# Performance work log

Measured on AMD Instinct MI355X. Metric: run time of the kernel, lower is better.

## Reference

```python
import jax, jax.numpy as jnp
import numpy as np

IN_CH = 128
HIDDEN = 256
CHUNK = 4096
EPS = 1e-8  # F.cosine_similarity default eps


def setup_inputs() -> dict:
    key = jax.random.key(0)
    ks = jax.random.split(key, 10)
    N, E, P = 8192, 262144, 65536
    x = jax.random.normal(ks[0], (N, IN_CH), dtype=jnp.float32)
    edge_index = jax.random.randint(ks[1], (2, E), 0, N, dtype=jnp.int64)
    edge_pairs = jax.random.randint(ks[2], (P, 2), 0, N, dtype=jnp.int64)
    input_dim = 2 * IN_CH + IN_CH + IN_CH + IN_CH + 1 + 3  # 644
    h2 = HIDDEN // 2
    def lin(k, fan_in, fan_out):
        bound = 1.0 / np.sqrt(fan_in)
        kw, kb = jax.random.split(k)
        W = jax.random.uniform(kw, (fan_in, fan_out), minval=-bound, maxval=bound, dtype=jnp.float32)
        b = jax.random.uniform(kb, (fan_out,), minval=-bound, maxval=bound, dtype=jnp.float32)
        return W, b
    W1, b1 = lin(ks[3], input_dim, HIDDEN)
    W2, b2 = lin(ks[4], HIDDEN, h2)
    W3, b3 = lin(ks[5], h2, 1)
    return {"x": x, "edge_index": edge_index, "edge_pairs": edge_pairs,
            "W1": W1, "b1": b1, "W2": W2, "b2": b2, "W3": W3, "b3": b3}


def _forward(x, edge_index, edge_pairs, W1, b1, W2, b2, W3, b3):
    N = x.shape[0]
    # dense adjacency cache (matches DenseHeuristicMixin._ensure_graph_cache)
    adj = jnp.zeros((N, N), dtype=jnp.float32).at[edge_index[0], edge_index[1]].set(1.0)
    diag = jnp.arange(N)
    adj = adj.at[diag, diag].set(0.0)
    deg = adj.sum(axis=1)
    inv_log_deg = jnp.where(deg > 1, 1.0 / jnp.log(jnp.where(deg > 1, deg, 2.0)), 0.0)
    inv_deg = jnp.where(deg > 0, 1.0 / jnp.where(deg > 0, deg, 1.0), 0.0)

    P = edge_pairs.shape[0]
    pairs = edge_pairs.reshape(P // CHUNK, CHUNK, 2)

    def chunk_body(carry, pc):
        u, v = pc[:, 0], pc[:, 1]
        xu, xv = x[u], x[v]                          # [C, d]
        # cosine similarity (eps-clamped denominator, as in torch)
        nu = jnp.sqrt(jnp.sum(xu * xu, axis=1))
        nv = jnp.sqrt(jnp.sum(xv * xv, axis=1))
        cos = jnp.sum(xu * xv, axis=1) / jnp.maximum(nu * nv, EPS)
        # dense heuristic features: [C, N] adjacency-row products
        common = adj[u] * adj[v]
        cn = common.sum(axis=1)
        aa = common @ inv_log_deg
        ra = common @ inv_deg
        feats = jnp.concatenate(
            [xu, xv, xu * xv, jnp.abs(xu - xv), xu + xv,
             cos[:, None], cn[:, None], aa[:, None], ra[:, None]], axis=1)
        h = jax.nn.relu(feats @ W1 + b1)  # dropout is identity in eval mode
        h = jax.nn.relu(h @ W2 + b2)
        s = (h @ W3 + b3)[:, 0]
        return carry, s

    _, scores = jax.lax.scan(chunk_body, None, pairs)
    return scores.reshape(-1)


def reference(x, edge_index, edge_pairs, W1, b1, W2, b2, W3, b3):
    return _forward(x, edge_index, edge_pairs, W1, b1, W2, b2, W3, b3)
```

## Files before the change

### kernel.cpp

```cpp
#include <hip/hip_runtime.h>
#include <hip/hip_bf16.h>

#define IN_CH   128
#define HIDDEN  256
#define H2DIM   128
#define KS1     17
#define KS2     8
#define NT1     16
#define NT2     8
#define FSTR    296
#define H1S     264
#define CAP     64
#define T1PACK  (NT1*KS1*64)
#define T2PACK  (NT2*KS2*64)

typedef short short8v __attribute__((ext_vector_type(8)));
typedef float f32x4   __attribute__((ext_vector_type(4)));

__device__ __forceinline__ ushort f2bf(float f) {
  union { float f; uint32_t u; } c; c.f = f;
  uint32_t u = c.u + 0x7FFFu + ((c.u >> 16) & 1u);
  return (ushort)(u >> 16);
}
__device__ __forceinline__ float bf2f(ushort h) {
  union { uint32_t u; float f; } c; c.u = ((uint32_t)h) << 16;
  return c.f;
}
__device__ __forceinline__ float bfLo(uint32_t u) { return bf2f((ushort)(u & 0xffffu)); }
__device__ __forceinline__ float bfHi(uint32_t u) { return bf2f((ushort)(u >> 16)); }
__device__ __forceinline__ uint32_t pk2(float a, float b) {
  __hip_bfloat162 h = __float22bfloat162_rn(make_float2(a, b));
  union { __hip_bfloat162 h; uint32_t u; } c; c.h = h;
  return c.u;
}

__global__ void k_prep(const float* __restrict__ W1, const float* __restrict__ W2,
                       ushort* __restrict__ w1p, ushort* __restrict__ w2p,
                       uint32_t* __restrict__ bits, int nwords) {
  int t = blockIdx.x * blockDim.x + threadIdx.x;
  if (t < T1PACK) {
    int l = t & 63;
    int rest = t >> 6;
    int ks = rest % KS1;
    int nt = rest / KS1;
    int n  = nt * 16 + (l & 15);
    int k0 = ks * 32 + (l >> 4) * 8;
    short8v v;
    #pragma unroll
    for (int j = 0; j < 8; ++j) {
      int k = k0 + j;
      float val;
      if (k < 128)      val = W1[(size_t)k * HIDDEN + n] + W1[(size_t)(512 + k) * HIDDEN + n];
      else if (k < 256) val = W1[(size_t)k * HIDDEN + n] + W1[(size_t)(384 + k) * HIDDEN + n];
      else if (k < 512) val = W1[(size_t)k * HIDDEN + n];
      else if (k < 516) val = W1[(size_t)(k + 128) * HIDDEN + n];
      else              val = 0.f;
      v[j] = (short)f2bf(val);
    }
    *(short8v*)(w1p + (size_t)t * 8) = v;
  } else if (t < T1PACK + T2PACK) {
    int t2 = t - T1PACK;
    int l = t2 & 63;
    int rest = t2 >> 6;
    int ks = rest % KS2;
    int nt = rest / KS2;
    int n  = nt * 16 + (l & 15);
    int k0 = ks * 32 + (l >> 4) * 8;
    short8v v;
    #pragma unroll
    for (int j = 0; j < 8; ++j)
      v[j] = (short)f2bf(W2[(size_t)(k0 + j) * H2DIM + n]);
    *(short8v*)(w2p + (size_t)t2 * 8) = v;
  }
  int stride = gridDim.x * blockDim.x;
  for (int i = t; i < nwords; i += stride) bits[i] = 0u;
}

__global__ void k_build_adj(const int* __restrict__ ei, int E, int roww,
                            uint32_t* __restrict__ bits) {
  int e = blockIdx.x * blockDim.x + threadIdx.x;
  if (e >= E) return;
  int u = ei[e];
  int v = ei[E + e];
  if (u == v) return;
  atomicOr((unsigned int*)&bits[(size_t)u * roww + (v >> 5)], 1u << (v & 31));
}

__global__ void k_node_lists(const uint32_t* __restrict__ bits, const float* __restrict__ x,
                             int nnodes, int roww,
                             float* __restrict__ invlog, float* __restrict__ invdeg,
                             int* __restrict__ deg, float* __restrict__ nrm,
                             ushort* __restrict__ adjl, ushort* __restrict__ xbf) {
  int node = blockIdx.x * (blockDim.x >> 6) + (threadIdx.x >> 6);
  int lane = threadIdx.x & 63;
  if (node >= nnodes) return;
  const uint32_t* row = bits + (size_t)node * roww;
  uint32_t wd[4];
  int c = 0;
  #pragma unroll
  for (int j = 0; j < 4; ++j) { wd[j] = row[lane * 4 + j]; c += __popc(wd[j]); }
  int sum = c;
  #pragma unroll
  for (int off = 1; off < 64; off <<= 1) {
    int t = __shfl_up(sum, off);
    if (lane >= off) sum += t;
  }
  int excl = sum - c;
  int total = __shfl(sum, 63);
  ushort* lst = adjl + (size_t)node * CAP;
  int pos = excl;
  #pragma unroll
  for (int j = 0; j < 4; ++j) {
    uint32_t m = wd[j];
    int base = (lane * 4 + j) * 32;
    while (m) {
      int b = __ffs(m) - 1;
      if (pos < CAP) lst[pos] = (ushort)(base + b);
      ++pos;
      m &= m - 1;
    }
  }
  float2 xa = *(const float2*)(x + (size_t)node * IN_CH + 2 * lane);
  *(uint32_t*)(xbf + (size_t)node * IN_CH + 2 * lane) = pk2(xa.x, xa.y);
  float ss = xa.x * xa.x + xa.y * xa.y;
  #pragma unroll
  for (int off = 32; off; off >>= 1) ss += __shfl_xor(ss, off);
  if (lane == 0) {
    deg[node] = total;
    float d = (float)total;
    invlog[node] = (total > 1) ? 1.0f / logf(d) : 0.0f;
    invdeg[node] = (total > 0) ? 1.0f / d : 0.0f;
    nrm[node] = sqrtf(ss);
  }
}

__global__ __launch_bounds__(512, 4) void k_mlp10(
    const ushort* __restrict__ xbf, const int* __restrict__ pairs,
    const uint32_t* __restrict__ bits, int roww,
    const int* __restrict__ deg, const float* __restrict__ nrm,
    const float* __restrict__ invlog, const float* __restrict__ invdeg,
    const ushort* __restrict__ adjl,
    const ushort* __restrict__ w1p, const float* __restrict__ b1,
    const ushort* __restrict__ w2p, const float* __restrict__ b2,
    const float* __restrict__ W3, const float* __restrict__ b3,
    float* __restrict__ out, int P)
{
  __shared__ ushort feats[64 * FSTR];
  __shared__ float outacc[64];
  __shared__ int us[64], vs[64];

  int tid = threadIdx.x;
  int pb = blockIdx.x * 64;
  int w  = tid >> 6, l = tid & 63;
  int pg = l >> 3, g = l & 7;
  int lr = l & 15;
  int lk = l >> 4;

  if (tid < 64) {
    int2 pr = ((const int2*)pairs)[pb + tid];
    us[tid] = pr.x; vs[tid] = pr.y;
    outacc[tid] = b3[0];
  }
  __syncthreads();

  int p = w * 8 + pg;
  int u = us[p], v = vs[p];
  ushort* fpR = feats + p * FSTR;
  ushort* fp  = fpR + g * 16;

  {
    const ushort* xup = xbf + (size_t)u * IN_CH + g * 16;
    const ushort* xvp = xbf + (size_t)v * IN_CH + g * 16;
    uint4 A0 = *(const uint4*)(xup);
    uint4 A1 = *(const uint4*)(xup + 8);
    uint4 B0 = *(const uint4*)(xvp);
    uint4 B1 = *(const uint4*)(xvp + 8);
    *(uint4*)(fp)       = A0;
    *(uint4*)(fp + 8)   = A1;
    *(uint4*)(fp + 128) = B0;
    *(uint4*)(fp + 136) = B1;
    float suv = bfLo(A0.x)*bfLo(B0.x) + bfHi(A0.x)*bfHi(B0.x)
              + bfLo(A0.y)*bfLo(B0.y) + bfHi(A0.y)*bfHi(B0.y)
              + bfLo(A0.z)*bfLo(B0.z) + bfHi(A0.z)*bfHi(B0.z)
              + bfLo(A0.w)*bfLo(B0.w) + bfHi(A0.w)*bfHi(B0.w)
              + bfLo(A1.x)*bfLo(B1.x) + bfHi(A1.x)*bfHi(B1.x)
              + bfLo(A1.y)*bfLo(B1.y) + bfHi(A1.y)*bfHi(B1.y)
              + bfLo(A1.z)*bfLo(B1.z) + bfHi(A1.z)*bfHi(B1.z)
              + bfLo(A1.w)*bfLo(B1.w) + bfHi(A1.w)*bfHi(B1.w);
    suv += __shfl_xor(suv, 1);
    suv += __shfl_xor(suv, 2);
    suv += __shfl_xor(suv, 4);
    if (g == 0) fpR[256] = f2bf(suv / fmaxf(nrm[u] * nrm[v], 1e-8f));
    if (g < 7) *(uint2*)(fpR + 260 + 4 * g) = make_uint2(0u, 0u);
  }

  {
    int sdmin[8], snbs[8];
    uint32_t swrd[8];
    bool sfall = false;
    #pragma unroll
    for (int pp = 0; pp < 8; ++pp) {
      int ps_ = w * 8 + pp;
      int uu = us[ps_], vv = vs[ps_];
      int du = deg[uu], dv = deg[vv];
      int nu = adjl[(size_t)uu * CAP + l];
      int nv = adjl[(size_t)vv * CAP + l];
      bool ule = du <= dv;
      sdmin[pp] = ule ? du : dv;
      int o  = ule ? vv : uu;
      int nb = (ule ? nu : nv) & 8191;
      snbs[pp] = nb;
      swrd[pp] = bits[(size_t)o * roww + (nb >> 5)];
      sfall |= (sdmin[pp] > CAP);
    }
    if (!sfall) {
      #pragma unroll
      for (int pp = 0; pp < 8; ++pp) {
        bool h = (l < sdmin[pp]) && ((swrd[pp] >> (snbs[pp] & 31)) & 1u);
        unsigned long long mask = __ballot(h);
        float cnv = (float)__popcll(mask);
        float aa = 0.f, ra = 0.f;
        if (mask) {
          float il = 0.f, ig = 0.f;
          if (h) { il = invlog[snbs[pp]]; ig = invdeg[snbs[pp]]; }
          while (mask) {
            int ln = __ffsll(mask) - 1;
            aa += __shfl(il, ln);
            ra += __shfl(ig, ln);
            mask &= mask - 1;
          }
        }
        if (l == 0) {
          ushort* fq = feats + (w * 8 + pp) * FSTR;
          fq[257] = f2bf(cnv); fq[258] = f2bf(aa); fq[259] = f2bf(ra);
        }
      }
    } else {
      for (int pp = 0; pp < 8; ++pp) {
        int ps_ = w * 8 + pp;
        int uu = us[ps_], vv = vs[ps_];
        float cnL = 0.f, aaL = 0.f, raL = 0.f;
        const uint32_t* ru = bits + (size_t)uu * roww;
        const uint32_t* rv = bits + (size_t)vv * roww;
        for (int wd = l; wd < roww; wd += 64) {
          uint32_t c = ru[wd] & rv[wd];
          cnL += (float)__popc(c);
          while (c) {
            int bb = __ffs(c) - 1;
            int idx = wd * 32 + bb;
            aaL += invlog[idx]; raL += invdeg[idx];
            c &= c - 1;
          }
        }
        #pragma unroll
        for (int off = 32; off; off >>= 1) {
          cnL += __shfl_xor(cnL, off);
          aaL += __shfl_xor(aaL, off);
          raL += __shfl_xor(raL, off);
        }
        if (l == 0) {
          ushort* fq = feats + (w * 8 + pp) * FSTR;
          fq[257] = f2bf(cnL); fq[258] = f2bf(aaL); fq[259] = f2bf(raL);
        }
      }
    }
  }
  __syncthreads();

  f32x4 acc[4][2];
  #pragma unroll
  for (int m = 0; m < 4; ++m)
    #pragma unroll
    for (int i = 0; i < 2; ++i) acc[m][i] = (f32x4){0.f, 0.f, 0.f, 0.f};

  const ushort* aB = feats + lr * FSTR + lk * 8;
  const ushort* bW = w1p + (size_t)(w * 2) * KS1 * 512 + l * 8;

  {
    short8v bf[2][2];
    #pragma unroll
    for (int i = 0; i < 2; ++i)
      bf[0][i] = *(const short8v*)(bW + (size_t)(i * KS1) * 512);
    #pragma unroll
    for (int ks = 0; ks < 8; ++ks) {
      int cur = ks & 1, nxt = cur ^ 1;
      if (ks + 1 < 8) {
        #pragma unroll
        for (int i = 0; i < 2; ++i)
          bf[nxt][i] = *(const short8v*)(bW + (size_t)(i * KS1 + ks + 1) * 512);
      }
      short8v am[4];
      #pragma unroll
      for (int m = 0; m < 4; ++m)
        am[m] = *(const short8v*)(aB + m * 16 * FSTR + ks * 32);
      #pragma unroll
      for (int i = 0; i < 2; ++i)
        #pragma unroll
        for (int m = 0; m < 4; ++m)
          acc[m][i] = __builtin_amdgcn_mfma_f32_16x16x32_bf16(am[m], bf[cur][i], acc[m][i], 0, 0, 0);
    }
  }
  __syncthreads();

  {
    uint4 A0 = *(uint4*)(fp);
    uint4 A1 = *(uint4*)(fp + 8);
    uint4 B0 = *(uint4*)(fp + 128);
    uint4 B1 = *(uint4*)(fp + 136);
    uint4 P0, P1, D0, D1;
    #define PD(Au, Bu, Pu, Du)                                                 \
      {                                                                        \
        float alo = bfLo(Au), ahi = bfHi(Au);                                  \
        float blo = bfLo(Bu), bhi = bfHi(Bu);                                  \
        Pu = pk2(alo * blo, ahi * bhi);                                        \
        Du = pk2(fabsf(alo - blo), fabsf(ahi - bhi));                          \
      }
    PD(A0.x, B0.x, P0.x, D0.x) PD(A0.y, B0.y, P0.y, D0.y)
    PD(A0.z, B0.z, P0.z, D0.z) PD(A0.w, B0.w, P0.w, D0.w)
    PD(A1.x, B1.x, P1.x, D1.x) PD(A1.y, B1.y, P1.y, D1.y)
    PD(A1.z, B1.z, P1.z, D1.z) PD(A1.w, B1.w, P1.w, D1.w)
    #undef PD
    *(uint4*)(fp)       = P0;
    *(uint4*)(fp + 8)   = P1;
    *(uint4*)(fp + 128) = D0;
    *(uint4*)(fp + 136) = D1;
  }
  __syncthreads();

  {
    short8v bf[2][2];
    #pragma unroll
    for (int i = 0; i < 2; ++i)
      bf[0][i] = *(const short8v*)(bW + (size_t)(i * KS1 + 8) * 512);
    #pragma unroll
    for (int ks = 8; ks < KS1; ++ks) {
      int cur = ks & 1, nxt = cur ^ 1;
      if (ks + 1 < KS1) {
        #pragma unroll
        for (int i = 0; i < 2; ++i)
          bf[nxt][i] = *(const short8v*)(bW + (size_t)(i * KS1 + ks + 1) * 512);
      }
      short8v am[4];
      #pragma unroll
      for (int m = 0; m < 4; ++m)
        am[m] = *(const short8v*)(aB + m * 16 * FSTR + (ks - 8) * 32);
      #pragma unroll
      for (int i = 0; i < 2; ++i)
        #pragma unroll
        for (int m = 0; m < 4; ++m)
          acc[m][i] = __builtin_amdgcn_mfma_f32_16x16x32_bf16(am[m], bf[cur][i], acc[m][i], 0, 0, 0);
    }
  }

  uint32_t h1r[2][8];
  #pragma unroll
  for (int i = 0; i < 2; ++i) {
    float bias = b1[(w * 2 + i) * 16 + lr];
    #pragma unroll
    for (int m = 0; m < 4; ++m) {
      float v0 = fmaxf(acc[m][i][0] + bias, 0.f);
      float v1 = fmaxf(acc[m][i][1] + bias, 0.f);
      float v2 = fmaxf(acc[m][i][2] + bias, 0.f);
      float v3 = fmaxf(acc[m][i][3] + bias, 0.f);
      h1r[i][m * 2]     = pk2(v0, v1);
      h1r[i][m * 2 + 1] = pk2(v2, v3);
    }
  }
  __syncthreads();

  ushort* h1 = feats;
  #pragma unroll
  for (int i = 0; i < 2; ++i) {
    int col = (w * 2 + i) * 16 + lr;
    #pragma unroll
    for (int m = 0; m < 4; ++m) {
      int row0 = m * 16 + lk * 4;
      h1[(row0)     * H1S + col] = (ushort)(h1r[i][m * 2]);
      h1[(row0 + 1) * H1S + col] = (ushort)(h1r[i][m * 2] >> 16);
      h1[(row0 + 2) * H1S + col] = (ushort)(h1r[i][m * 2 + 1]);
      h1[(row0 + 3) * H1S + col] = (ushort)(h1r[i][m * 2 + 1] >> 16);
    }
  }
  __syncthreads();

  f32x4 acc2[4];
  #pragma unroll
  for (int m = 0; m < 4; ++m) acc2[m] = (f32x4){0.f, 0.f, 0.f, 0.f};

  const ushort* aB2 = h1 + lr * H1S + lk * 8;
  const ushort* bW2 = w2p + (size_t)w * KS2 * 512 + l * 8;

  short8v b2f[2];
  b2f[0] = *(const short8v*)(bW2);

  #pragma unroll
  for (int ks = 0; ks < KS2; ++ks) {
    int cur = ks & 1, nxt = cur ^ 1;
    if (ks + 1 < KS2)
      b2f[nxt] = *(const short8v*)(bW2 + (size_t)(ks + 1) * 512);
    #pragma unroll
    for (int m = 0; m < 4; ++m) {
      short8v am = *(const short8v*)(aB2 + m * 16 * H1S + ks * 32);
      acc2[m] = __builtin_amdgcn_mfma_f32_16x16x32_bf16(am, b2f[cur], acc2[m], 0, 0, 0);
    }
  }

  {
    int col = w * 16 + lr;
    float bias = b2[col];
    float w3v = W3[col];
    #pragma unroll
    for (int m = 0; m < 4; ++m) {
      #pragma unroll
      for (int r = 0; r < 4; ++r) {
        float h = fmaxf(acc2[m][r] + bias, 0.f) * w3v;
        h += __shfl_xor(h, 1);
        h += __shfl_xor(h, 2);
        h += __shfl_xor(h, 4);
        h += __shfl_xor(h, 8);
        if (lr == 0) atomicAdd(&outacc[m * 16 + lk * 4 + r], h);
      }
    }
  }
  __syncthreads();

  if (tid < 64) out[pb + tid] = outacc[tid];
}

extern "C" void kernel_launch(void* const* d_in, const int* in_sizes, int n_in,
                              void* d_out, int out_size, void* d_ws, size_t ws_size,
                              hipStream_t stream) {
  const float* x     = (const float*)d_in[0];
  const int*   ei    = (const int*)d_in[1];
  const int*   pairs = (const int*)d_in[2];
  const float* W1    = (const float*)d_in[3];
  const float* b1    = (const float*)d_in[4];
  const float* W2    = (const float*)d_in[5];
  const float* b2    = (const float*)d_in[6];
  const float* W3    = (const float*)d_in[7];
  const float* b3    = (const float*)d_in[8];
  float* out = (float*)d_out;

  int N = in_sizes[0] / IN_CH;
  int E = in_sizes[1] / 2;
  int P = in_sizes[2] / 2;
  int roww = (N + 31) >> 5;

  char* wsb = (char*)d_ws;
  uint32_t* bits = (uint32_t*)wsb;                       size_t off = (size_t)N * roww * 4;
  float* invlog  = (float*)(wsb + off);                  off += (size_t)N * 4;
  float* invdeg  = (float*)(wsb + off);                  off += (size_t)N * 4;
  int*   deg     = (int*)(wsb + off);                    off += (size_t)N * 4;
  float* nrm     = (float*)(wsb + off);                  off += (size_t)N * 4;
  ushort* adjl   = (ushort*)(wsb + off);                 off += (size_t)N * CAP * 2;
  ushort* xbf    = (ushort*)(wsb + off);                 off += (size_t)N * IN_CH * 2;
  ushort* w1pack = (ushort*)(wsb + off);                 off += (size_t)T1PACK * 8 * 2;
  ushort* w2pack = (ushort*)(wsb + off);                 off += (size_t)T2PACK * 8 * 2;

  int nwords = N * roww;
  k_prep<<<1024, 256, 0, stream>>>(W1, W2, w1pack, w2pack, bits, nwords);
  k_build_adj<<<(E + 255) / 256, 256, 0, stream>>>(ei, E, roww, bits);
  k_node_lists<<<(N + 3) / 4, 256, 0, stream>>>(bits, x, N, roww, invlog, invdeg, deg, nrm, adjl, xbf);
  k_mlp10<<<P / 64, 512, 0, stream>>>(xbf, pairs, bits, roww, deg, nrm, invlog, invdeg, adjl,
                                      w1pack, b1, w2pack, b2, W3, b3, out, P);
}
```

Baseline: 79.23 us.

## Intersect sorted neighbor lists via warp binary search, pack node scalars into float2

Common-neighbor features now come from intersecting the two sorted adjacency lists inside a wavefront with a shuffle-based binary search when both degrees fit the cap, which avoids the random bitmap word gathers. The bitmap probe remains as a middle fallback and a full bitmap scan as the last resort. Per-node degree and norm, and the two inverse-degree terms, are packed into float2 arrays so each needs one load instead of two. The per-pair loop is no longer unrolled across 8 pairs, which reduces batching of the global loads.

```diff
diff --git a/kernel.cpp b/kernel.cpp
--- a/kernel.cpp
+++ b/kernel.cpp
@@ -88,8 +88,7 @@
 
 __global__ void k_node_lists(const uint32_t* __restrict__ bits, const float* __restrict__ x,
                              int nnodes, int roww,
-                             float* __restrict__ invlog, float* __restrict__ invdeg,
-                             int* __restrict__ deg, float* __restrict__ nrm,
+                             float2* __restrict__ dn, float2* __restrict__ nodeinv,
                              ushort* __restrict__ adjl, ushort* __restrict__ xbf) {
   int node = blockIdx.x * (blockDim.x >> 6) + (threadIdx.x >> 6);
   int lane = threadIdx.x & 63;
@@ -126,19 +125,18 @@
   #pragma unroll
   for (int off = 32; off; off >>= 1) ss += __shfl_xor(ss, off);
   if (lane == 0) {
-    deg[node] = total;
     float d = (float)total;
-    invlog[node] = (total > 1) ? 1.0f / logf(d) : 0.0f;
-    invdeg[node] = (total > 0) ? 1.0f / d : 0.0f;
-    nrm[node] = sqrtf(ss);
-  }
-}
-
-__global__ __launch_bounds__(512, 4) void k_mlp10(
+    dn[node] = make_float2(d, sqrtf(ss));
+    float il = (total > 1) ? 1.0f / logf(d) : 0.0f;
+    float ig = (total > 0) ? 1.0f / d : 0.0f;
+    nodeinv[node] = make_float2(il, ig);
+  }
+}
+
+__global__ __launch_bounds__(512, 4) void k_mlp11(
     const ushort* __restrict__ xbf, const int* __restrict__ pairs,
     const uint32_t* __restrict__ bits, int roww,
-    const int* __restrict__ deg, const float* __restrict__ nrm,
-    const float* __restrict__ invlog, const float* __restrict__ invdeg,
+    const float2* __restrict__ dn, const float2* __restrict__ nodeinv,
     const ushort* __restrict__ adjl,
     const ushort* __restrict__ w1p, const float* __restrict__ b1,
     const ushort* __restrict__ w2p, const float* __restrict__ b2,
@@ -190,79 +188,89 @@
     suv += __shfl_xor(suv, 1);
     suv += __shfl_xor(suv, 2);
     suv += __shfl_xor(suv, 4);
-    if (g == 0) fpR[256] = f2bf(suv / fmaxf(nrm[u] * nrm[v], 1e-8f));
+    if (g == 0) {
+      float nu = dn[u].y, nv = dn[v].y;
+      fpR[256] = f2bf(suv / fmaxf(nu * nv, 1e-8f));
+    }
     if (g < 7) *(uint2*)(fpR + 260 + 4 * g) = make_uint2(0u, 0u);
   }
 
-  {
-    int sdmin[8], snbs[8];
-    uint32_t swrd[8];
-    bool sfall = false;
-    #pragma unroll
-    for (int pp = 0; pp < 8; ++pp) {
-      int ps_ = w * 8 + pp;
-      int uu = us[ps_], vv = vs[ps_];
-      int du = deg[uu], dv = deg[vv];
-      int nu = adjl[(size_t)uu * CAP + l];
-      int nv = adjl[(size_t)vv * CAP + l];
-      bool ule = du <= dv;
-      sdmin[pp] = ule ? du : dv;
-      int o  = ule ? vv : uu;
-      int nb = (ule ? nu : nv) & 8191;
-      snbs[pp] = nb;
-      swrd[pp] = bits[(size_t)o * roww + (nb >> 5)];
-      sfall |= (sdmin[pp] > CAP);
-    }
-    if (!sfall) {
-      #pragma unroll
-      for (int pp = 0; pp < 8; ++pp) {
-        bool h = (l < sdmin[pp]) && ((swrd[pp] >> (snbs[pp] & 31)) & 1u);
-        unsigned long long mask = __ballot(h);
-        float cnv = (float)__popcll(mask);
-        float aa = 0.f, ra = 0.f;
-        if (mask) {
-          float il = 0.f, ig = 0.f;
-          if (h) { il = invlog[snbs[pp]]; ig = invdeg[snbs[pp]]; }
-          while (mask) {
-            int ln = __ffsll(mask) - 1;
-            aa += __shfl(il, ln);
-            ra += __shfl(ig, ln);
-            mask &= mask - 1;
-          }
+  for (int pp = 0; pp < 8; ++pp) {
+    int ps_ = w * 8 + pp;
+    int uu = us[ps_], vv = vs[ps_];
+    int du = (int)dn[uu].x, dv = (int)dn[vv].x;
+    bool ule = du <= dv;
+    int sn = ule ? uu : vv, on = ule ? vv : uu;
+    int ds = ule ? du : dv, dl = ule ? dv : du;
+    float cnv, aa = 0.f, ra = 0.f;
+    if (dl <= CAP) {
+      int a = adjl[(size_t)sn * CAP + l];
+      int b = adjl[(size_t)on * CAP + l];
+      int pos = 0;
+      #pragma unroll
+      for (int st = 32; st; st >>= 1) {
+        int cand = pos + st;
+        int bv = __shfl(b, cand - 1);
+        if (cand <= dl && bv < a) pos = cand;
+      }
+      int bp = __shfl(b, pos);
+      bool hit = (l < ds) && (pos < dl) && (bp == a);
+      unsigned long long mask = __ballot(hit);
+      cnv = (float)__popcll(mask);
+      if (mask) {
+        float il = 0.f, ig = 0.f;
+        if (hit) { float2 nv = nodeinv[a]; il = nv.x; ig = nv.y; }
+        while (mask) {
+          int ln = __ffsll(mask) - 1;
+          aa += __shfl(il, ln);
+          ra += __shfl(ig, ln);
+          mask &= mask - 1;
         }
-        if (l == 0) {
-          ushort* fq = feats + (w * 8 + pp) * FSTR;
-          fq[257] = f2bf(cnv); fq[258] = f2bf(aa); fq[259] = f2bf(ra);
+      }
+    } else if (ds <= CAP) {
+      bool hit = false; int nb = 0;
+      if (l < ds) {
+        nb = adjl[(size_t)sn * CAP + l];
+        hit = (bits[(size_t)on * roww + (nb >> 5)] >> (nb & 31)) & 1u;
+      }
+      unsigned long long mask = __ballot(hit);
+      cnv = (float)__popcll(mask);
+      if (mask) {
+        float il = 0.f, ig = 0.f;
+        if (hit) { float2 nv = nodeinv[nb]; il = nv.x; ig = nv.y; }
+        while (mask) {
+          int ln = __ffsll(mask) - 1;
+          aa += __shfl(il, ln);
+          ra += __shfl(ig, ln);
+          mask &= mask - 1;
         }
       }
     } else {
-      for (int pp = 0; pp < 8; ++pp) {
-        int ps_ = w * 8 + pp;
-        int uu = us[ps_], vv = vs[ps_];
-        float cnL = 0.f, aaL = 0.f, raL = 0.f;
-        const uint32_t* ru = bits + (size_t)uu * roww;
-        const uint32_t* rv = bits + (size_t)vv * roww;
-        for (int wd = l; wd < roww; wd += 64) {
-          uint32_t c = ru[wd] & rv[wd];
-          cnL += (float)__popc(c);
-          while (c) {
-            int bb = __ffs(c) - 1;
-            int idx = wd * 32 + bb;
-            aaL += invlog[idx]; raL += invdeg[idx];
-            c &= c - 1;
-          }
+      float cnL = 0.f, aaL = 0.f, raL = 0.f;
+      const uint32_t* ru = bits + (size_t)uu * roww;
+      const uint32_t* rv = bits + (size_t)vv * roww;
+      for (int wd = l; wd < roww; wd += 64) {
+        uint32_t c = ru[wd] & rv[wd];
+        cnL += (float)__popc(c);
+        while (c) {
+          int bb = __ffs(c) - 1;
+          int idx = wd * 32 + bb;
+          float2 nv = nodeinv[idx];
+          aaL += nv.x; raL += nv.y;
+          c &= c - 1;
         }
-        #pragma unroll
-        for (int off = 32; off; off >>= 1) {
-          cnL += __shfl_xor(cnL, off);
-          aaL += __shfl_xor(aaL, off);
-          raL += __shfl_xor(raL, off);
-        }
-        if (l == 0) {
-          ushort* fq = feats + (w * 8 + pp) * FSTR;
-          fq[257] = f2bf(cnL); fq[258] = f2bf(aaL); fq[259] = f2bf(raL);
-        }
-      }
+      }
+      #pragma unroll
+      for (int off = 32; off; off >>= 1) {
+        cnL += __shfl_xor(cnL, off);
+        aaL += __shfl_xor(aaL, off);
+        raL += __shfl_xor(raL, off);
+      }
+      cnv = cnL; aa = aaL; ra = raL;
+    }
+    if (l == 0) {
+      ushort* fq = feats + ps_ * FSTR;
+      fq[257] = f2bf(cnv); fq[258] = f2bf(aa); fq[259] = f2bf(ra);
     }
   }
   __syncthreads();
@@ -447,20 +455,18 @@
   int roww = (N + 31) >> 5;
 
   char* wsb = (char*)d_ws;
-  uint32_t* bits = (uint32_t*)wsb;                       size_t off = (size_t)N * roww * 4;
-  float* invlog  = (float*)(wsb + off);                  off += (size_t)N * 4;
-  float* invdeg  = (float*)(wsb + off);                  off += (size_t)N * 4;
-  int*   deg     = (int*)(wsb + off);                    off += (size_t)N * 4;
-  float* nrm     = (float*)(wsb + off);                  off += (size_t)N * 4;
-  ushort* adjl   = (ushort*)(wsb + off);                 off += (size_t)N * CAP * 2;
-  ushort* xbf    = (ushort*)(wsb + off);                 off += (size_t)N * IN_CH * 2;
-  ushort* w1pack = (ushort*)(wsb + off);                 off += (size_t)T1PACK * 8 * 2;
-  ushort* w2pack = (ushort*)(wsb + off);                 off += (size_t)T2PACK * 8 * 2;
+  uint32_t* bits   = (uint32_t*)wsb;                     size_t off = (size_t)N * roww * 4;
+  float2* dn       = (float2*)(wsb + off);               off += (size_t)N * 8;
+  float2* nodeinv  = (float2*)(wsb + off);               off += (size_t)N * 8;
+  ushort* adjl     = (ushort*)(wsb + off);               off += (size_t)N * CAP * 2;
+  ushort* xbf      = (ushort*)(wsb + off);               off += (size_t)N * IN_CH * 2;
+  ushort* w1pack   = (ushort*)(wsb + off);               off += (size_t)T1PACK * 8 * 2;
+  ushort* w2pack   = (ushort*)(wsb + off);               off += (size_t)T2PACK * 8 * 2;
 
   int nwords = N * roww;
   k_prep<<<1024, 256, 0, stream>>>(W1, W2, w1pack, w2pack, bits, nwords);
   k_build_adj<<<(E + 255) / 256, 256, 0, stream>>>(ei, E, roww, bits);
-  k_node_lists<<<(N + 3) / 4, 256, 0, stream>>>(bits, x, N, roww, invlog, invdeg, deg, nrm, adjl, xbf);
-  k_mlp10<<<P / 64, 512, 0, stream>>>(xbf, pairs, bits, roww, deg, nrm, invlog, invdeg, adjl,
+  k_node_lists<<<(N + 3) / 4, 256, 0, stream>>>(bits, x, N, roww, dn, nodeinv, adjl, xbf);
+  k_mlp11<<<P / 64, 512, 0, stream>>>(xbf, pairs, bits, roww, dn, nodeinv, adjl,
                                       w1pack, b1, w2pack, b2, W3, b3, out, P);
 }
```

Result: no change. 80.06 us (+1.1%).
